# Optimization experiments

Hardware: AMD Instinct MI355X
Metric: run time of the kernel (lower is better)

Reference implementation:

```python
import jax, jax.numpy as jnp
import numpy as np

TEMPERATURE = 8.0  # sqrt(d_k), d_k = 64


def setup_inputs() -> dict:
    key = jax.random.key(0)
    kq, kk, kv = jax.random.split(key, 3)
    BH, N, D = 16, 4096, 64  # batch*heads, seq_len, head_dim
    q = jax.random.normal(kq, (BH, N, D), dtype=jnp.float32)
    k = jax.random.normal(kk, (BH, N, D), dtype=jnp.float32)
    v = jax.random.normal(kv, (BH, N, D), dtype=jnp.float32)
    # causal mask: True means masked (filled with -inf), broadcast over BH
    mask = jnp.triu(jnp.ones((N, N), dtype=jnp.bool_), k=1)[None, :, :]
    return {"q": q, "k": k, "v": v, "mask": mask}


def reference(q, k, v, mask):
    # attn = q @ k^T / temperature, masked softmax, attn @ v
    scores = jnp.einsum("bnd,bmd->bnm", q, k) / TEMPERATURE
    scores = jnp.where(mask, -jnp.inf, scores)
    attn = jax.nn.softmax(scores, axis=-1)  # dropout p=0 (eval) -> identity
    out = jnp.einsum("bnm,bmd->bnd", attn, v)
    return out, attn
```

## Files before the change

kernel.cpp:

```cpp
#include <hip/hip_runtime.h>

typedef float f32x4 __attribute__((ext_vector_type(4)));
typedef __bf16 bf16x8 __attribute__((ext_vector_type(8)));
typedef unsigned short u16x8 __attribute__((ext_vector_type(8)));
typedef unsigned int u32x4 __attribute__((ext_vector_type(4)));

#define NBH 16
#define NSEQ 4096
#define DH 64

__device__ __forceinline__ unsigned int cvtpk(float lo, float hi) {
  unsigned int r;
  asm("v_cvt_pk_bf16_f32 %0, %1, %2" : "=v"(r) : "v"(lo), "v"(hi));
  return r;
}
__device__ __forceinline__ bf16x8 pk8(const float* f) {
  union { unsigned int u[4]; bf16x8 b; } x;
#pragma unroll
  for (int i = 0; i < 4; ++i) x.u[i] = cvtpk(f[2 * i], f[2 * i + 1]);
  return x.b;
}

__global__ __launch_bounds__(512, 4) void sdpa_fused(
    const float* __restrict__ qg, const float* __restrict__ kg,
    const float* __restrict__ vg, float* __restrict__ outg) {
  const int bid = blockIdx.x;
  const int xcd = bid & 7;
  const int idx = bid >> 3;
  const int hh = idx >> 5;
  const int b = 2 * xcd + hh;
  const int tt = idx & 31;
  const int qt2 = hh ? tt : (31 - tt);
  const int qr0 = qt2 * 128;
  const int nkt = 2 * (qt2 + 1);

  const int tid = threadIdx.x;
  const int w = tid >> 6, lane = tid & 63;
  const int g = lane >> 4, c = lane & 15;
  const int wr0 = 16 * w;

  const float* qb = qg + (size_t)b * NSEQ * DH;
  const float* kb = kg + (size_t)b * NSEQ * DH;
  const float* vb = vg + (size_t)b * NSEQ * DH;
  float* outb = outg + (size_t)b * NSEQ * DH;
  float* attnb = outg + (size_t)NBH * NSEQ * DH + (size_t)b * NSEQ * NSEQ;

  __shared__ unsigned short Kl[2][64][72];
  __shared__ unsigned int Vt[2][64][37];
  __shared__ unsigned short Pl[128][72];

  bf16x8 aq[2];
  {
    const float* qrow = qb + (size_t)(qr0 + wr0 + c) * DH;
#pragma unroll
    for (int ks = 0; ks < 2; ++ks) {
      float f[8];
      *(float4*)f = *(const float4*)(qrow + 32 * ks + 8 * g);
      *(float4*)(f + 4) = *(const float4*)(qrow + 32 * ks + 8 * g + 4);
      aq[ks] = pk8(f);
    }
  }

  const int kj = tid >> 3, kcs = tid & 7;
  const int vp = tid >> 4, dch = tid & 15;
  float kf[8], vf0[4], vf1[4];

  auto loadK = [&](int kt) {
    const float* s = kb + (size_t)(kt * 64 + kj) * DH + kcs * 8;
    *(float4*)kf = ((const float4*)s)[0];
    *(float4*)(kf + 4) = ((const float4*)s)[1];
  };
  auto writeK = [&](int cur) {
    u32x4 u;
#pragma unroll
    for (int i = 0; i < 4; ++i) u[i] = cvtpk(kf[2 * i], kf[2 * i + 1]);
    *(u32x4*)&Kl[cur][kj][kcs * 8] = u;
  };
  auto loadV = [&](int kt) {
    const float* s0 = vb + (size_t)(kt * 64 + 2 * vp) * DH + dch * 4;
    *(float4*)vf0 = *(const float4*)s0;
    *(float4*)vf1 = *(const float4*)(s0 + DH);
  };
  auto writeV = [&](int cur) {
#pragma unroll
    for (int e = 0; e < 4; ++e) Vt[cur][4 * dch + e][vp] = cvtpk(vf0[e], vf1[e]);
  };

  float part[4] = {0.f, 0.f, 0.f, 0.f};
  loadK(0);
  for (int kt = 0; kt < nkt; ++kt) {
    const int cur = kt & 1;
    writeK(cur);
    __syncthreads();
    if (kt + 1 < nkt) loadK(kt + 1);
    f32x4 acc[4];
#pragma unroll
    for (int ct = 0; ct < 4; ++ct) acc[ct] = (f32x4){0.f, 0.f, 0.f, 0.f};
#pragma unroll
    for (int ks = 0; ks < 2; ++ks)
#pragma unroll
      for (int ct = 0; ct < 4; ++ct) {
        u16x8 u = *(const u16x8*)&Kl[cur][16 * ct + c][32 * ks + 8 * g];
        acc[ct] = __builtin_amdgcn_mfma_f32_16x16x32_bf16(aq[ks], __builtin_bit_cast(bf16x8, u), acc[ct], 0, 0, 0);
      }
#pragma unroll
    for (int ct = 0; ct < 4; ++ct)
#pragma unroll
      for (int r = 0; r < 4; ++r) {
        const int j = kt * 64 + 16 * ct + c;
        const int i = qr0 + wr0 + 4 * g + r;
        part[r] += (j <= i) ? __expf(acc[ct][r] * 0.125f) : 0.f;
      }
  }
  float rinv[4];
#pragma unroll
  for (int r = 0; r < 4; ++r) {
    float s = part[r];
    s += __shfl_xor(s, 1); s += __shfl_xor(s, 2);
    s += __shfl_xor(s, 4); s += __shfl_xor(s, 8);
    rinv[r] = 1.f / s;
  }

  loadK(0);
  loadV(0);
  f32x4 oacc[4];
#pragma unroll
  for (int ct = 0; ct < 4; ++ct) oacc[ct] = (f32x4){0.f, 0.f, 0.f, 0.f};

  for (int kt = 0; kt < nkt; ++kt) {
    const int cur = kt & 1;
    writeK(cur);
    writeV(cur);
    __syncthreads();
    if (kt + 1 < nkt) { loadK(kt + 1); loadV(kt + 1); }

    f32x4 acc[4];
#pragma unroll
    for (int ct = 0; ct < 4; ++ct) acc[ct] = (f32x4){0.f, 0.f, 0.f, 0.f};
#pragma unroll
    for (int ks = 0; ks < 2; ++ks)
#pragma unroll
      for (int ct = 0; ct < 4; ++ct) {
        u16x8 u = *(const u16x8*)&Kl[cur][16 * ct + c][32 * ks + 8 * g];
        acc[ct] = __builtin_amdgcn_mfma_f32_16x16x32_bf16(aq[ks], __builtin_bit_cast(bf16x8, u), acc[ct], 0, 0, 0);
      }

#pragma unroll
    for (int ct = 0; ct < 4; ++ct)
#pragma unroll
      for (int r = 0; r < 4; ++r) {
        const int il = wr0 + 4 * g + r;
        const int jl = 16 * ct + c;
        const int i = qr0 + il;
        const int j = kt * 64 + jl;
        const float p = (j <= i) ? __expf(acc[ct][r] * 0.125f) * rinv[r] : 0.f;
        Pl[il][jl] = (unsigned short)cvtpk(p, p);
        attnb[(size_t)i * NSEQ + j] = p;
      }

    bf16x8 ap[2];
#pragma unroll
    for (int ks = 0; ks < 2; ++ks)
      ap[ks] = __builtin_bit_cast(bf16x8, *(const u16x8*)&Pl[wr0 + c][32 * ks + 8 * g]);
#pragma unroll
    for (int ks = 0; ks < 2; ++ks)
#pragma unroll
      for (int ct = 0; ct < 4; ++ct) {
        u16x8 bv = *(const u16x8*)&Vt[cur][16 * ct + c][16 * ks + 4 * g];
        oacc[ct] = __builtin_amdgcn_mfma_f32_16x16x32_bf16(ap[ks], __builtin_bit_cast(bf16x8, bv), oacc[ct], 0, 0, 0);
      }
  }

#pragma unroll
  for (int ct = 0; ct < 4; ++ct)
#pragma unroll
    for (int r = 0; r < 4; ++r) {
      const int i = qr0 + wr0 + 4 * g + r;
      outb[(size_t)i * DH + 16 * ct + c] = oacc[ct][r];
    }

  const int zc0 = 128 * (qt2 + 1);
  if (zc0 < NSEQ) {
    const int zw4 = (NSEQ - zc0) >> 2;
    const float4 z = {0.f, 0.f, 0.f, 0.f};
    for (int r = 0; r < 128; ++r) {
      float4* dst = (float4*)(attnb + (size_t)(qr0 + r) * NSEQ + zc0);
      for (int c4 = tid; c4 < zw4; c4 += 512) dst[c4] = z;
    }
  }
}

extern "C" void kernel_launch(void* const* d_in, const int* in_sizes, int n_in,
                              void* d_out, int out_size, void* d_ws, size_t ws_size,
                              hipStream_t stream) {
  (void)in_sizes; (void)n_in; (void)out_size; (void)d_ws; (void)ws_size;
  const float* q = (const float*)d_in[0];
  const float* k = (const float*)d_in[1];
  const float* v = (const float*)d_in[2];
  float* out = (float*)d_out;
  sdpa_fused<<<dim3(512), dim3(512), 0, stream>>>(q, k, v, out);
}
```

Before: 330.6 us.

## Pair complementary 64-row query tiles per block for causal load balance

Each block now handles two 64-row query tiles, qt and 63-qt, with half the waves on each, so every block walks the same number of key tiles and the causal work is balanced. Both groups share the K/V tiles staged in shared memory, and waves assigned to the shorter tile skip compute once past their diagonal. Synchronisation is replaced with a lighter LDS-only wait plus s_barrier. The cost is idle waves in the shorter group during later iterations and the K/V loads they no longer need.

```diff
diff --git a/kernel.cpp b/kernel.cpp
--- a/kernel.cpp
+++ b/kernel.cpp
@@ -19,6 +19,13 @@
 #pragma unroll
   for (int i = 0; i < 4; ++i) x.u[i] = cvtpk(f[2 * i], f[2 * i + 1]);
   return x.b;
+}
+
+__device__ __forceinline__ void lbar() {
+  __builtin_amdgcn_sched_barrier(0);
+  asm volatile("s_waitcnt lgkmcnt(0)" ::: "memory");
+  __builtin_amdgcn_s_barrier();
+  __builtin_amdgcn_sched_barrier(0);
 }
 
 __global__ __launch_bounds__(512, 4) void sdpa_fused(
@@ -26,22 +33,24 @@
     const float* __restrict__ vg, float* __restrict__ outg) {
   const int bid = blockIdx.x;
   const int xcd = bid & 7;
-  const int idx = bid >> 3;
-  const int hh = idx >> 5;
+  const int ii = bid >> 3;
+  const int hh = ii >> 5;
+  const int qt = ii & 31;
   const int b = 2 * xcd + hh;
-  const int tt = idx & 31;
-  const int qt2 = hh ? tt : (31 - tt);
-  const int qr0 = qt2 * 128;
-  const int nkt = 2 * (qt2 + 1);
+  const int qa = qt, qb = 63 - qt;
 
   const int tid = threadIdx.x;
   const int w = tid >> 6, lane = tid & 63;
   const int g = lane >> 4, c = lane & 15;
-  const int wr0 = 16 * w;
-
-  const float* qb = qg + (size_t)b * NSEQ * DH;
-  const float* kb = kg + (size_t)b * NSEQ * DH;
-  const float* vb = vg + (size_t)b * NSEQ * DH;
+  const int grp = w >> 2;
+  const int wr0 = 16 * (w & 3);
+  const int qrw = (grp ? qb : qa) * 64;
+  const int kmax = grp ? qb : qa;
+  const int pOff = 16 * w;
+
+  const float* qbp = qg + (size_t)b * NSEQ * DH;
+  const float* kbp = kg + (size_t)b * NSEQ * DH;
+  const float* vbp = vg + (size_t)b * NSEQ * DH;
   float* outb = outg + (size_t)b * NSEQ * DH;
   float* attnb = outg + (size_t)NBH * NSEQ * DH + (size_t)b * NSEQ * NSEQ;
 
@@ -51,7 +60,7 @@
 
   bf16x8 aq[2];
   {
-    const float* qrow = qb + (size_t)(qr0 + wr0 + c) * DH;
+    const float* qrow = qbp + (size_t)(qrw + wr0 + c) * DH;
 #pragma unroll
     for (int ks = 0; ks < 2; ++ks) {
       float f[8];
@@ -66,7 +75,7 @@
   float kf[8], vf0[4], vf1[4];
 
   auto loadK = [&](int kt) {
-    const float* s = kb + (size_t)(kt * 64 + kj) * DH + kcs * 8;
+    const float* s = kbp + (size_t)(kt * 64 + kj) * DH + kcs * 8;
     *(float4*)kf = ((const float4*)s)[0];
     *(float4*)(kf + 4) = ((const float4*)s)[1];
   };
@@ -77,7 +86,7 @@
     *(u32x4*)&Kl[cur][kj][kcs * 8] = u;
   };
   auto loadV = [&](int kt) {
-    const float* s0 = vb + (size_t)(kt * 64 + 2 * vp) * DH + dch * 4;
+    const float* s0 = vbp + (size_t)(kt * 64 + 2 * vp) * DH + dch * 4;
     *(float4*)vf0 = *(const float4*)s0;
     *(float4*)vf1 = *(const float4*)(s0 + DH);
   };
@@ -88,29 +97,31 @@
 
   float part[4] = {0.f, 0.f, 0.f, 0.f};
   loadK(0);
-  for (int kt = 0; kt < nkt; ++kt) {
+  for (int kt = 0; kt <= qb; ++kt) {
     const int cur = kt & 1;
     writeK(cur);
-    __syncthreads();
-    if (kt + 1 < nkt) loadK(kt + 1);
-    f32x4 acc[4];
-#pragma unroll
-    for (int ct = 0; ct < 4; ++ct) acc[ct] = (f32x4){0.f, 0.f, 0.f, 0.f};
-#pragma unroll
-    for (int ks = 0; ks < 2; ++ks)
-#pragma unroll
-      for (int ct = 0; ct < 4; ++ct) {
-        u16x8 u = *(const u16x8*)&Kl[cur][16 * ct + c][32 * ks + 8 * g];
-        acc[ct] = __builtin_amdgcn_mfma_f32_16x16x32_bf16(aq[ks], __builtin_bit_cast(bf16x8, u), acc[ct], 0, 0, 0);
-      }
-#pragma unroll
-    for (int ct = 0; ct < 4; ++ct)
-#pragma unroll
-      for (int r = 0; r < 4; ++r) {
-        const int j = kt * 64 + 16 * ct + c;
-        const int i = qr0 + wr0 + 4 * g + r;
-        part[r] += (j <= i) ? __expf(acc[ct][r] * 0.125f) : 0.f;
-      }
+    lbar();
+    if (kt < qb) loadK(kt + 1);
+    if (kt <= kmax) {
+      f32x4 acc[4];
+#pragma unroll
+      for (int ct = 0; ct < 4; ++ct) acc[ct] = (f32x4){0.f, 0.f, 0.f, 0.f};
+#pragma unroll
+      for (int ks = 0; ks < 2; ++ks)
+#pragma unroll
+        for (int ct = 0; ct < 4; ++ct) {
+          u16x8 u = *(const u16x8*)&Kl[cur][16 * ct + c][32 * ks + 8 * g];
+          acc[ct] = __builtin_amdgcn_mfma_f32_16x16x32_bf16(aq[ks], __builtin_bit_cast(bf16x8, u), acc[ct], 0, 0, 0);
+        }
+#pragma unroll
+      for (int ct = 0; ct < 4; ++ct)
+#pragma unroll
+        for (int r = 0; r < 4; ++r) {
+          const int j = kt * 64 + 16 * ct + c;
+          const int i = qrw + wr0 + 4 * g + r;
+          part[r] += (j <= i) ? __expf(acc[ct][r] * 0.125f) : 0.f;
+        }
+    }
   }
   float rinv[4];
 #pragma unroll
@@ -121,71 +132,78 @@
     rinv[r] = 1.f / s;
   }
 
+  __syncthreads();
+
   loadK(0);
   loadV(0);
   f32x4 oacc[4];
 #pragma unroll
   for (int ct = 0; ct < 4; ++ct) oacc[ct] = (f32x4){0.f, 0.f, 0.f, 0.f};
 
-  for (int kt = 0; kt < nkt; ++kt) {
+  for (int kt = 0; kt <= qb; ++kt) {
     const int cur = kt & 1;
     writeK(cur);
     writeV(cur);
-    __syncthreads();
-    if (kt + 1 < nkt) { loadK(kt + 1); loadV(kt + 1); }
-
-    f32x4 acc[4];
-#pragma unroll
-    for (int ct = 0; ct < 4; ++ct) acc[ct] = (f32x4){0.f, 0.f, 0.f, 0.f};
-#pragma unroll
-    for (int ks = 0; ks < 2; ++ks)
-#pragma unroll
-      for (int ct = 0; ct < 4; ++ct) {
-        u16x8 u = *(const u16x8*)&Kl[cur][16 * ct + c][32 * ks + 8 * g];
-        acc[ct] = __builtin_amdgcn_mfma_f32_16x16x32_bf16(aq[ks], __builtin_bit_cast(bf16x8, u), acc[ct], 0, 0, 0);
+    lbar();
+    if (kt < qb) { loadK(kt + 1); loadV(kt + 1); }
+
+    if (kt <= kmax) {
+      f32x4 acc[4];
+#pragma unroll
+      for (int ct = 0; ct < 4; ++ct) acc[ct] = (f32x4){0.f, 0.f, 0.f, 0.f};
+#pragma unroll
+      for (int ks = 0; ks < 2; ++ks)
+#pragma unroll
+        for (int ct = 0; ct < 4; ++ct) {
+          u16x8 u = *(const u16x8*)&Kl[cur][16 * ct + c][32 * ks + 8 * g];
+          acc[ct] = __builtin_amdgcn_mfma_f32_16x16x32_bf16(aq[ks], __builtin_bit_cast(bf16x8, u), acc[ct], 0, 0, 0);
+        }
+
+#pragma unroll
+      for (int ct = 0; ct < 4; ++ct)
+#pragma unroll
+        for (int r = 0; r < 4; ++r) {
+          const int jl = 16 * ct + c;
+          const int i = qrw + wr0 + 4 * g + r;
+          const int j = kt * 64 + jl;
+          const float p = (j <= i) ? __expf(acc[ct][r] * 0.125f) * rinv[r] : 0.f;
+          Pl[pOff + 4 * g + r][jl] = (unsigned short)cvtpk(p, p);
+          attnb[(size_t)i * NSEQ + j] = p;
+        }
+
+      bf16x8 ap[2];
+#pragma unroll
+      for (int ks = 0; ks < 2; ++ks)
+        ap[ks] = __builtin_bit_cast(bf16x8, *(const u16x8*)&Pl[pOff + c][32 * ks + 8 * g]);
+#pragma unroll
+      for (int ks = 0; ks < 2; ++ks)
+#pragma unroll
+        for (int ct = 0; ct < 4; ++ct) {
+          u16x8 bv = *(const u16x8*)&Vt[cur][16 * ct + c][16 * ks + 4 * g];
+          oacc[ct] = __builtin_amdgcn_mfma_f32_16x16x32_bf16(ap[ks], __builtin_bit_cast(bf16x8, bv), oacc[ct], 0, 0, 0);
+        }
+    }
+  }
+
+#pragma unroll
+  for (int ct = 0; ct < 4; ++ct)
+#pragma unroll
+    for (int r = 0; r < 4; ++r) {
+      const int i = qrw + wr0 + 4 * g + r;
+      outb[(size_t)i * DH + 16 * ct + c] = oacc[ct][r];
+    }
+
+  const float4 z = {0.f, 0.f, 0.f, 0.f};
+#pragma unroll
+  for (int t = 0; t < 2; ++t) {
+    const int q0 = t ? qb : qa;
+    const int zc0 = 64 * (q0 + 1);
+    if (zc0 < NSEQ) {
+      const int zw4 = (NSEQ - zc0) >> 2;
+      for (int r = 0; r < 64; ++r) {
+        float4* dst = (float4*)(attnb + (size_t)(q0 * 64 + r) * NSEQ + zc0);
+        for (int c4 = tid; c4 < zw4; c4 += 512) dst[c4] = z;
       }
-
-#pragma unroll
-    for (int ct = 0; ct < 4; ++ct)
-#pragma unroll
-      for (int r = 0; r < 4; ++r) {
-        const int il = wr0 + 4 * g + r;
-        const int jl = 16 * ct + c;
-        const int i = qr0 + il;
-        const int j = kt * 64 + jl;
-        const float p = (j <= i) ? __expf(acc[ct][r] * 0.125f) * rinv[r] : 0.f;
-        Pl[il][jl] = (unsigned short)cvtpk(p, p);
-        attnb[(size_t)i * NSEQ + j] = p;
-      }
-
-    bf16x8 ap[2];
-#pragma unroll
-    for (int ks = 0; ks < 2; ++ks)
-      ap[ks] = __builtin_bit_cast(bf16x8, *(const u16x8*)&Pl[wr0 + c][32 * ks + 8 * g]);
-#pragma unroll
-    for (int ks = 0; ks < 2; ++ks)
-#pragma unroll
-      for (int ct = 0; ct < 4; ++ct) {
-        u16x8 bv = *(const u16x8*)&Vt[cur][16 * ct + c][16 * ks + 4 * g];
-        oacc[ct] = __builtin_amdgcn_mfma_f32_16x16x32_bf16(ap[ks], __builtin_bit_cast(bf16x8, bv), oacc[ct], 0, 0, 0);
-      }
-  }
-
-#pragma unroll
-  for (int ct = 0; ct < 4; ++ct)
-#pragma unroll
-    for (int r = 0; r < 4; ++r) {
-      const int i = qr0 + wr0 + 4 * g + r;
-      outb[(size_t)i * DH + 16 * ct + c] = oacc[ct][r];
-    }
-
-  const int zc0 = 128 * (qt2 + 1);
-  if (zc0 < NSEQ) {
-    const int zw4 = (NSEQ - zc0) >> 2;
-    const float4 z = {0.f, 0.f, 0.f, 0.f};
-    for (int r = 0; r < 128; ++r) {
-      float4* dst = (float4*)(attnb + (size_t)(qr0 + r) * NSEQ + zc0);
-      for (int c4 = tid; c4 < zw4; c4 += 512) dst[c4] = z;
     }
   }
 }
```

New measurement: 324.4 us. About the same (-1.9%).

## Halve query tile to 64 rows, double block count, single-buffer V

Applied to the files above, without the earlier changes.

Each block now handles 64 query rows with 256 threads (4 waves) instead of 128 rows with 512 threads, and the grid grows from 512 to 1024 blocks. Tile assignment pairs a short and a long causal tile inside each block-index range to balance work across XCDs. V is single-buffered, with an extra barrier at the end of each iteration. A lighter barrier (waitcnt on LDS only plus s_barrier) replaces __syncthreads. The smaller blocks should improve occupancy and load balance, at the cost of more barriers per tile and K/V being reloaded twice as often per query row.

```diff
diff --git a/kernel.cpp b/kernel.cpp
--- a/kernel.cpp
+++ b/kernel.cpp
@@ -21,37 +21,44 @@
   return x.b;
 }
 
-__global__ __launch_bounds__(512, 4) void sdpa_fused(
+__device__ __forceinline__ void lbar() {
+  __builtin_amdgcn_sched_barrier(0);
+  asm volatile("s_waitcnt lgkmcnt(0)" ::: "memory");
+  __builtin_amdgcn_s_barrier();
+  __builtin_amdgcn_sched_barrier(0);
+}
+
+__global__ __launch_bounds__(256, 4) void sdpa_fused(
     const float* __restrict__ qg, const float* __restrict__ kg,
     const float* __restrict__ vg, float* __restrict__ outg) {
   const int bid = blockIdx.x;
   const int xcd = bid & 7;
-  const int idx = bid >> 3;
-  const int hh = idx >> 5;
+  const int ii = bid >> 3;
+  const int hh = ii >> 6;
+  const int tt = ii & 63;
+  const int qt = (tt < 32) ? tt : 95 - tt;
   const int b = 2 * xcd + hh;
-  const int tt = idx & 31;
-  const int qt2 = hh ? tt : (31 - tt);
-  const int qr0 = qt2 * 128;
-  const int nkt = 2 * (qt2 + 1);
+  const int qr0 = qt * 64;
+  const int nkt = qt + 1;
 
   const int tid = threadIdx.x;
   const int w = tid >> 6, lane = tid & 63;
   const int g = lane >> 4, c = lane & 15;
   const int wr0 = 16 * w;
 
-  const float* qb = qg + (size_t)b * NSEQ * DH;
-  const float* kb = kg + (size_t)b * NSEQ * DH;
-  const float* vb = vg + (size_t)b * NSEQ * DH;
+  const float* qbp = qg + (size_t)b * NSEQ * DH;
+  const float* kbp = kg + (size_t)b * NSEQ * DH;
+  const float* vbp = vg + (size_t)b * NSEQ * DH;
   float* outb = outg + (size_t)b * NSEQ * DH;
   float* attnb = outg + (size_t)NBH * NSEQ * DH + (size_t)b * NSEQ * NSEQ;
 
   __shared__ unsigned short Kl[2][64][72];
-  __shared__ unsigned int Vt[2][64][37];
-  __shared__ unsigned short Pl[128][72];
+  __shared__ unsigned int Vt[64][37];
+  __shared__ unsigned short Pl[64][72];
 
   bf16x8 aq[2];
   {
-    const float* qrow = qb + (size_t)(qr0 + wr0 + c) * DH;
+    const float* qrow = qbp + (size_t)(qr0 + wr0 + c) * DH;
 #pragma unroll
     for (int ks = 0; ks < 2; ++ks) {
       float f[8];
@@ -61,29 +68,30 @@
     }
   }
 
-  const int kj = tid >> 3, kcs = tid & 7;
-  const int vp = tid >> 4, dch = tid & 15;
-  float kf[8], vf0[4], vf1[4];
+  const int kj = tid >> 2, kcs = tid & 3;
+  const int vp = tid >> 3, vch = tid & 7;
+  float kf[16], vf0[8], vf1[8];
 
   auto loadK = [&](int kt) {
-    const float* s = kb + (size_t)(kt * 64 + kj) * DH + kcs * 8;
-    *(float4*)kf = ((const float4*)s)[0];
-    *(float4*)(kf + 4) = ((const float4*)s)[1];
+    const float* s = kbp + (size_t)(kt * 64 + kj) * DH + kcs * 16;
+#pragma unroll
+    for (int i = 0; i < 4; ++i) *(float4*)(kf + 4 * i) = ((const float4*)s)[i];
   };
   auto writeK = [&](int cur) {
-    u32x4 u;
-#pragma unroll
-    for (int i = 0; i < 4; ++i) u[i] = cvtpk(kf[2 * i], kf[2 * i + 1]);
-    *(u32x4*)&Kl[cur][kj][kcs * 8] = u;
+    unsigned int* dst = (unsigned int*)&Kl[cur][kj][kcs * 16];
+#pragma unroll
+    for (int i = 0; i < 8; ++i) dst[i] = cvtpk(kf[2 * i], kf[2 * i + 1]);
   };
   auto loadV = [&](int kt) {
-    const float* s0 = vb + (size_t)(kt * 64 + 2 * vp) * DH + dch * 4;
-    *(float4*)vf0 = *(const float4*)s0;
-    *(float4*)vf1 = *(const float4*)(s0 + DH);
-  };
-  auto writeV = [&](int cur) {
-#pragma unroll
-    for (int e = 0; e < 4; ++e) Vt[cur][4 * dch + e][vp] = cvtpk(vf0[e], vf1[e]);
+    const float* s0 = vbp + (size_t)(kt * 64 + 2 * vp) * DH + vch * 8;
+    *(float4*)vf0 = ((const float4*)s0)[0];
+    *(float4*)(vf0 + 4) = ((const float4*)s0)[1];
+    *(float4*)vf1 = ((const float4*)(s0 + DH))[0];
+    *(float4*)(vf1 + 4) = ((const float4*)(s0 + DH))[1];
+  };
+  auto writeV = [&]() {
+#pragma unroll
+    for (int e = 0; e < 8; ++e) Vt[vch * 8 + e][vp] = cvtpk(vf0[e], vf1[e]);
   };
 
   float part[4] = {0.f, 0.f, 0.f, 0.f};
@@ -91,7 +99,7 @@
   for (int kt = 0; kt < nkt; ++kt) {
     const int cur = kt & 1;
     writeK(cur);
-    __syncthreads();
+    lbar();
     if (kt + 1 < nkt) loadK(kt + 1);
     f32x4 acc[4];
 #pragma unroll
@@ -121,6 +129,8 @@
     rinv[r] = 1.f / s;
   }
 
+  __syncthreads();
+
   loadK(0);
   loadV(0);
   f32x4 oacc[4];
@@ -130,8 +140,8 @@
   for (int kt = 0; kt < nkt; ++kt) {
     const int cur = kt & 1;
     writeK(cur);
-    writeV(cur);
-    __syncthreads();
+    writeV();
+    lbar();
     if (kt + 1 < nkt) { loadK(kt + 1); loadV(kt + 1); }
 
     f32x4 acc[4];
@@ -149,12 +159,11 @@
     for (int ct = 0; ct < 4; ++ct)
 #pragma unroll
       for (int r = 0; r < 4; ++r) {
-        const int il = wr0 + 4 * g + r;
         const int jl = 16 * ct + c;
-        const int i = qr0 + il;
+        const int i = qr0 + wr0 + 4 * g + r;
         const int j = kt * 64 + jl;
         const float p = (j <= i) ? __expf(acc[ct][r] * 0.125f) * rinv[r] : 0.f;
-        Pl[il][jl] = (unsigned short)cvtpk(p, p);
+        Pl[wr0 + 4 * g + r][jl] = (unsigned short)cvtpk(p, p);
         attnb[(size_t)i * NSEQ + j] = p;
       }
 
@@ -166,9 +175,10 @@
     for (int ks = 0; ks < 2; ++ks)
 #pragma unroll
       for (int ct = 0; ct < 4; ++ct) {
-        u16x8 bv = *(const u16x8*)&Vt[cur][16 * ct + c][16 * ks + 4 * g];
+        u16x8 bv = *(const u16x8*)&Vt[16 * ct + c][16 * ks + 4 * g];
         oacc[ct] = __builtin_amdgcn_mfma_f32_16x16x32_bf16(ap[ks], __builtin_bit_cast(bf16x8, bv), oacc[ct], 0, 0, 0);
       }
+    lbar();
   }
 
 #pragma unroll
@@ -179,13 +189,13 @@
       outb[(size_t)i * DH + 16 * ct + c] = oacc[ct][r];
     }
 
-  const int zc0 = 128 * (qt2 + 1);
+  const int zc0 = 64 * (qt + 1);
   if (zc0 < NSEQ) {
     const int zw4 = (NSEQ - zc0) >> 2;
     const float4 z = {0.f, 0.f, 0.f, 0.f};
-    for (int r = 0; r < 128; ++r) {
+    for (int r = 0; r < 64; ++r) {
       float4* dst = (float4*)(attnb + (size_t)(qr0 + r) * NSEQ + zc0);
-      for (int c4 = tid; c4 < zw4; c4 += 512) dst[c4] = z;
+      for (int c4 = tid; c4 < zw4; c4 += 256) dst[c4] = z;
     }
   }
 }
@@ -198,5 +208,5 @@
   const float* k = (const float*)d_in[1];
   const float* v = (const float*)d_in[2];
   float* out = (float*)d_out;
-  sdpa_fused<<<dim3(512), dim3(512), 0, stream>>>(q, k, v, out);
-}
+  sdpa_fused<<<dim3(1024), dim3(256), 0, stream>>>(q, k, v, out);
+}
```

Measured after the change: 349.0 us. 1.06x slower.
